# Kernel tuning notes

Hardware: AMD Instinct MI355X
Metric: run time of the kernel (lower is better)

The kernel has to match this reference:

```python
import jax, jax.numpy as jnp
import numpy as np

N, T, D = 32, 64, 16
F = 512  # object_classes == feature dim after object_fc


def _gcn(x, adj, W, b):
    # Kipf GraphConvolution: adj @ (x @ W) + b
    return adj @ (x @ W) + b


def _norm_adj(a):
    d = jnp.sum(a, axis=1) ** -0.5
    return a * d[:, None] * d[None, :]


def _per_graph(x, gc1_W, gc1_b, gc2_W, gc2_b, gc3_W, gc3_b, gc4_W, gc4_b):
    # x: [D, F]
    # graph_generator / adj2: softmax-style similarity adjacency with D^{-1/2} norm
    s = x @ x.T                                   # [D, D]
    a = jnp.exp(s - jnp.max(s, axis=1, keepdims=True))
    adj = _norm_adj(a)
    # branch 1
    x1 = jax.nn.relu(_gcn(x, adj, gc1_W, gc1_b))
    x1 = _gcn(x1, adj, gc2_W, gc2_b)
    # branch 2 (adj_hat2 identical construction from x)
    y2 = jax.nn.relu(_gcn(x, adj, gc3_W, gc3_b))  # [D, 32]
    y22 = y2 @ y2.T
    nrm = jnp.sqrt(jnp.sum(y22 * y22, axis=1, keepdims=True))  # torch.norm(y22, 2, dim=1)
    adj3 = 1.0 + y22 / (nrm @ nrm.T)
    adj_hat3 = _norm_adj(adj3)
    y2 = _gcn(y2, adj_hat3, gc4_W, gc4_b)
    return (x1 + y2) * 0.5


def setup_inputs() -> dict:
    key = jax.random.key(0)
    ks = jax.random.split(key, 12)
    s = 0.02
    return {
        "object_raw": jax.random.normal(ks[0], (N * T * D, F), jnp.float32),
        "action_raw": jax.random.normal(ks[1], (N * T, F), jnp.float32),
        "W_obj": jax.random.normal(ks[2], (F, 512), jnp.float32) * s,
        "b_obj": jnp.zeros((512,), jnp.float32),
        "W_act": jax.random.normal(ks[3], (F, 512), jnp.float32) * s,
        "b_act": jnp.zeros((512,), jnp.float32),
        "gc1_W": jax.random.normal(ks[4], (512, 32), jnp.float32) * s,
        "gc1_b": jnp.zeros((32,), jnp.float32),
        "gc2_W": jax.random.normal(ks[5], (32, 512), jnp.float32) * s,
        "gc2_b": jnp.zeros((512,), jnp.float32),
        "gc3_W": jax.random.normal(ks[6], (512, 32), jnp.float32) * s,
        "gc3_b": jnp.zeros((32,), jnp.float32),
        "gc4_W": jax.random.normal(ks[7], (32, 512), jnp.float32) * s,
        "gc4_b": jnp.zeros((512,), jnp.float32),
        "fc1_W": jax.random.normal(ks[8], (512, 1024), jnp.float32) * s,
        "fc1_b": jnp.zeros((1024,), jnp.float32),
        "clf_W": jax.random.normal(ks[9], (1024, 500), jnp.float32) * s,
        "clf_b": jnp.zeros((500,), jnp.float32),
    }


def reference(object_raw, action_raw, W_obj, b_obj, W_act, b_act,
              gc1_W, gc1_b, gc2_W, gc2_b, gc3_W, gc3_b, gc4_W, gc4_b,
              fc1_W, fc1_b, clf_W, clf_b):
    obj = jax.nn.relu(object_raw @ W_obj + b_obj).reshape(N * T, D, 512)
    act = jax.nn.relu(action_raw @ W_act + b_act)           # [N*T, 512]
    obj = obj.at[:, D // 2].set(act)                         # overwrite middle frame
    graph = jax.vmap(lambda x: _per_graph(x, gc1_W, gc1_b, gc2_W, gc2_b,
                                          gc3_W, gc3_b, gc4_W, gc4_b))(obj)
    g = graph.reshape(N, T, D, 512).mean(axis=2)
    o = obj.reshape(N, T, D, 512).mean(axis=2)
    feat = (o + g) * 0.5                                     # graph_fusion == 'mean'
    c = jax.nn.relu(feat)                                    # dropout = identity (eval)
    c = jax.nn.relu(c @ fc1_W + fc1_b)
    out = (c @ clf_W + clf_b).mean(axis=1)                   # mean over T -> [N, 500]
    return out
```

## Files before the change

### kernel.cpp

```cpp
#include <hip/hip_runtime.h>
#include <hip/hip_bf16.h>

using ushort_t = unsigned short;
using f32x4  = __attribute__((ext_vector_type(4))) float;
using short8 = __attribute__((ext_vector_type(8))) short;

__device__ __forceinline__ float bflo(unsigned p) {
    union { unsigned u; float f; } x; x.u = p << 16; return x.f;
}
__device__ __forceinline__ float bfhi(unsigned p) {
    union { unsigned u; float f; } x; x.u = p & 0xffff0000u; return x.f;
}
__device__ __forceinline__ ushort_t f2bf(float f) {
    __hip_bfloat16 h = __float2bfloat16(f);
    return *(ushort_t*)&h;
}
__device__ __forceinline__ unsigned pk2bf(float lo, float hi) {
    __hip_bfloat162 h = __float22bfloat162_rn({lo, hi});
    return *(unsigned*)&h;
}

__device__ __forceinline__ void tr_tile(const float* __restrict__ S, ushort_t* __restrict__ D,
                                        int K, int N, int Npad, int bx, int by,
                                        int tx, int ty, float* tile )
{
    const int k0 = by * 32, n0 = bx * 32;
#pragma unroll
    for (int r = 0; r < 4; r++) {
        const int k = k0 + ty + r * 8, n = n0 + tx;
        tile[(ty + r * 8) * 33 + tx] = (k < K && n < N) ? S[(size_t)k * N + n] : 0.f;
    }
    __syncthreads();
#pragma unroll
    for (int r = 0; r < 4; r++) {
        const int n = n0 + ty + r * 8, k = k0 + tx;
        if (n < Npad && k < K) D[(size_t)n * K + k] = f2bf(tile[tx * 33 + ty + r * 8]);
    }
}

__global__ __launch_bounds__(256)
void prep_weights(const float* __restrict__ Wobj, ushort_t* __restrict__ WobjT,
                  const float* __restrict__ Wact, ushort_t* __restrict__ WactT,
                  const float* __restrict__ fc1W, ushort_t* __restrict__ fc1T,
                  const float* __restrict__ gc1W, ushort_t* __restrict__ W1t,
                  const float* __restrict__ gc3W, ushort_t* __restrict__ W3t,
                  const float* __restrict__ gc2W, ushort_t* __restrict__ W2bf,
                  const float* __restrict__ gc4W, ushort_t* __restrict__ W4bf)
{
    __shared__ float tile[32 * 33];
    const int b = blockIdx.x;
    const int t = threadIdx.x;
    const int tx = t & 31, ty = t >> 5;

    if (b < 1056) {
        const float* S; ushort_t* D; int K, N, Npad, nt, l;
        if      (b < 256)  { S = Wobj; D = WobjT; K = 512; N = 512;  Npad = 512;  nt = 16; l = b; }
        else if (b < 512)  { S = Wact; D = WactT; K = 512; N = 512;  Npad = 512;  nt = 16; l = b - 256; }
        else if (b < 1024) { S = fc1W; D = fc1T;  K = 512; N = 1024; Npad = 1024; nt = 32; l = b - 512; }
        else if (b < 1040) { S = gc1W; D = W1t;   K = 512; N = 32;   Npad = 32;   nt = 1;  l = b - 1024; }
        else               { S = gc3W; D = W3t;   K = 512; N = 32;   Npad = 32;   nt = 1;  l = b - 1040; }
        tr_tile(S, D, K, N, Npad, l % nt, l / nt, tx, ty, tile);
    } else {
        const float* S = (b < 1064) ? gc2W : gc4W;
        ushort_t* D    = (b < 1064) ? W2bf : W4bf;
        const int i = (b < 1064 ? b - 1056 : b - 1064) * 256 + t;
        const float4 x = ((const float4*)S)[2 * i];
        const float4 y = ((const float4*)S)[2 * i + 1];
        unsigned r[4] = { pk2bf(x.x, x.y), pk2bf(x.z, x.w), pk2bf(y.x, y.y), pk2bf(y.z, y.w) };
        ((uint4*)D)[i] = *(uint4*)r;
    }
}

__global__ __launch_bounds__(512, 4)
void gemm_obj_stream(const float* __restrict__ A, const ushort_t* __restrict__ Bt,
                     const float* __restrict__ bias, ushort_t* __restrict__ C)
{
    __shared__ __align__(16) ushort_t As[64 * 512];
    const int t = threadIdx.x;
    const int lane = t & 63, w = t >> 6;
    const int bm = blockIdx.x * 64;
    const int fr = lane & 15, fq = lane >> 4;

#pragma unroll
    for (int i = 0; i < 8; i++) {
        const int flat = i * 512 + t;
        const int row = flat >> 6, c = flat & 63;
        const float* gp = A + (size_t)(bm + row) * 512 + c * 8;
        const float4 p0 = *(const float4*)gp;
        const float4 p1 = *(const float4*)(gp + 4);
        unsigned rr[4] = { pk2bf(p0.x, p0.y), pk2bf(p0.z, p0.w),
                           pk2bf(p1.x, p1.y), pk2bf(p1.z, p1.w) };
        *(uint4*)&As[row * 512 + ((c ^ (row & 7)) * 8)] = *(uint4*)rr;
    }
    __syncthreads();

    const int nw = w * 64;
    const ushort_t* Bbase = Bt + (size_t)(nw + fr) * 512 + fq * 8;

    f32x4 acc[4][4];
#pragma unroll
    for (int j = 0; j < 4; j++)
#pragma unroll
        for (int i = 0; i < 4; i++) acc[j][i] = (f32x4){0.f, 0.f, 0.f, 0.f};

    uint4 bA[4], bB[4];
#pragma unroll
    for (int j = 0; j < 4; j++) bA[j] = *(const uint4*)(Bbase + (size_t)j * 16 * 512);

    for (int kk = 0; kk < 16; kk += 2) {
        short8 af[4];
#pragma unroll
        for (int i = 0; i < 4; i++)
            af[i] = *(const short8*)&As[(i * 16 + fr) * 512 + (((kk * 4 + fq) ^ (fr & 7)) * 8)];
#pragma unroll
        for (int j = 0; j < 4; j++) {
            bB[j] = *(const uint4*)(Bbase + (size_t)j * 16 * 512 + (kk + 1) * 32);
            const short8 bf = *(const short8*)&bA[j];
#pragma unroll
            for (int i = 0; i < 4; i++)
                acc[j][i] = __builtin_amdgcn_mfma_f32_16x16x32_bf16(af[i], bf, acc[j][i], 0, 0, 0);
        }
#pragma unroll
        for (int i = 0; i < 4; i++)
            af[i] = *(const short8*)&As[(i * 16 + fr) * 512 + ((((kk + 1) * 4 + fq) ^ (fr & 7)) * 8)];
#pragma unroll
        for (int j = 0; j < 4; j++) {
            if (kk + 2 < 16)
                bA[j] = *(const uint4*)(Bbase + (size_t)j * 16 * 512 + (kk + 2) * 32);
            const short8 bf = *(const short8*)&bB[j];
#pragma unroll
            for (int i = 0; i < 4; i++)
                acc[j][i] = __builtin_amdgcn_mfma_f32_16x16x32_bf16(af[i], bf, acc[j][i], 0, 0, 0);
        }
    }

#pragma unroll
    for (int j = 0; j < 4; j++) {
        const int n = nw + j * 16 + fr;
        const float bv = bias[n];
#pragma unroll
        for (int i = 0; i < 4; i++) {
#pragma unroll
            for (int rr = 0; rr < 4; rr++) {
                const int ml = fq * 4 + rr;
                if (ml == 8) continue;
                const int m = bm + i * 16 + ml;
                C[(size_t)m * 512 + n] = f2bf(fmaxf(acc[j][i][rr] + bv, 0.f));
            }
        }
    }
}

typedef __attribute__((address_space(1))) void glb_void;
typedef __attribute__((address_space(3))) void lds_void;
__device__ __forceinline__ void dma16(const void* g, void* l) {
    __builtin_amdgcn_global_load_lds((glb_void*)(unsigned long long)(uintptr_t)g,
                                     (lds_void*)(unsigned)(uintptr_t)l, 16, 0, 0);
}

template<int RELU, typename AT>
__global__ __launch_bounds__(256)
void gemm_dma(const AT* __restrict__ A, const ushort_t* __restrict__ Bt,
              const float* __restrict__ bias, ushort_t* __restrict__ C,
              int N, int K, int Nb, int row_mul, int row_add)
{
    __shared__ __align__(16) char     AsRaw[128 * 32 * sizeof(AT)];
    __shared__ __align__(16) ushort_t Bs[128 * 32];
    const int t = threadIdx.x;
    const int lane = t & 63, w = t >> 6;
    const int bm = blockIdx.y * 128, bn = blockIdx.x * 128;
    const int mb = (w & 1) * 64, nb = (w >> 1) * 64;
    const int fr = lane & 15, fq = lane >> 4;

    f32x4 acc[16];
#pragma unroll
    for (int i = 0; i < 16; i++) acc[i] = (f32x4){0.f, 0.f, 0.f, 0.f};

    const int brow = lane >> 2, bk = lane & 3;
    const int klog = bk ^ ((brow >> 1) & 3);
    const int arow = lane >> 3, ag = lane & 7;

    for (int k0 = 0; k0 < K; k0 += 32) {
        __syncthreads();
        if constexpr (sizeof(AT) == 4) {
#pragma unroll
            for (int i = 0; i < 4; i++) {
                const int grp = w * 4 + i;
                const int row = grp * 8 + arow;
                const int gl = ag ^ (row & 7);
                dma16((const float*)A + (size_t)(bm + row) * K + k0 + gl * 4,
                      AsRaw + grp * 1024);
            }
        } else {
#pragma unroll
            for (int i = 0; i < 2; i++) {
                const int grp = w * 2 + i;
                const int row = grp * 16 + brow;
                dma16((const ushort_t*)A + (size_t)(bm + row) * K + k0 + klog * 8,
                      (ushort_t*)AsRaw + grp * 512);
            }
        }
#pragma unroll
        for (int i = 0; i < 2; i++) {
            const int grp = w * 2 + i;
            const int row = grp * 16 + brow;
            dma16(Bt + (size_t)(bn + row) * K + k0 + klog * 8, Bs + grp * 512);
        }
        __syncthreads();

        short8 af[4], bf[4];
        if constexpr (sizeof(AT) == 4) {
#pragma unroll
            for (int i = 0; i < 4; i++) {
                const int row = mb + i * 16 + fr;
                const float* base = (const float*)AsRaw + row * 32;
                const f32x4 p0 = *(const f32x4*)(base + (((2 * fq)     ^ (fr & 7)) * 4));
                const f32x4 p1 = *(const f32x4*)(base + (((2 * fq + 1) ^ (fr & 7)) * 4));
                unsigned rr[4] = { pk2bf(p0.x, p0.y), pk2bf(p0.z, p0.w),
                                   pk2bf(p1.x, p1.y), pk2bf(p1.z, p1.w) };
                af[i] = *(short8*)rr;
            }
        } else {
#pragma unroll
            for (int i = 0; i < 4; i++) {
                const int row = mb + i * 16 + fr;
                af[i] = *(const short8*)((const ushort_t*)AsRaw + row * 32 + (fq ^ ((fr >> 1) & 3)) * 8);
            }
        }
#pragma unroll
        for (int j = 0; j < 4; j++) {
            const int row = nb + j * 16 + fr;
            bf[j] = *(const short8*)(Bs + row * 32 + (fq ^ ((fr >> 1) & 3)) * 8);
        }
#pragma unroll
        for (int i = 0; i < 4; i++)
#pragma unroll
            for (int j = 0; j < 4; j++)
                acc[i * 4 + j] = __builtin_amdgcn_mfma_f32_16x16x32_bf16(
                    af[i], bf[j], acc[i * 4 + j], 0, 0, 0);
    }

#pragma unroll
    for (int j = 0; j < 4; j++) {
        const int n = bn + nb + j * 16 + fr;
        const float bv = (n < Nb) ? bias[n] : 0.f;
#pragma unroll
        for (int i = 0; i < 4; i++) {
            const f32x4 a = acc[i * 4 + j];
#pragma unroll
            for (int r = 0; r < 4; r++) {
                const int m = bm + mb + i * 16 + fq * 4 + r;
                float v = a[r] + bv;
                if (RELU) v = fmaxf(v, 0.f);
                C[((size_t)m * row_mul + row_add) * (size_t)N + n] = f2bf(v);
            }
        }
    }
}

__global__ __launch_bounds__(64)
void graph_mfma(const ushort_t* __restrict__ obj,
                const ushort_t* __restrict__ W1t, const float* __restrict__ b1,
                const ushort_t* __restrict__ W2b, const float* __restrict__ b2,
                const ushort_t* __restrict__ W3t, const float* __restrict__ b3,
                const ushort_t* __restrict__ W4b, const float* __restrict__ b4,
                ushort_t* __restrict__ cbuf)
{
    __shared__ float ssb[16 * 17];
    __shared__ float adjt[16 * 20];
    __shared__ float t1s[16 * 36];
    __shared__ float t3s[16 * 36];
    __shared__ float x1s[16 * 36];
    __shared__ float y2s[16 * 36];
    __shared__ float y22s[16 * 17];
    __shared__ float a3t[16 * 20];
    __shared__ float dv[16], dv3[16], nrm[16], cA[16], cA3[16];
    __shared__ float zc1[32], zc4[32];

    const int lane = threadIdx.x;
    const int r = lane & 15, fq = lane >> 4;
    const ushort_t* xg = obj + (size_t)blockIdx.x * 8192;

    short8 xf[16];
#pragma unroll
    for (int kk = 0; kk < 16; kk++)
        xf[kk] = *(const short8*)(xg + r * 512 + kk * 32 + fq * 8);

    f32x4 sacc = (f32x4){0.f, 0.f, 0.f, 0.f};
#pragma unroll
    for (int kk = 0; kk < 16; kk++)
        sacc = __builtin_amdgcn_mfma_f32_16x16x32_bf16(xf[kk], xf[kk], sacc, 0, 0, 0);

    f32x4 a10 = (f32x4){0.f,0.f,0.f,0.f}, a11 = a10, a30 = a10, a31 = a10;
#pragma unroll
    for (int kk = 0; kk < 16; kk++) {
        const short8 w10 = *(const short8*)(W1t + (size_t)(r)      * 512 + kk * 32 + fq * 8);
        const short8 w11 = *(const short8*)(W1t + (size_t)(16 + r) * 512 + kk * 32 + fq * 8);
        const short8 w30 = *(const short8*)(W3t + (size_t)(r)      * 512 + kk * 32 + fq * 8);
        const short8 w31 = *(const short8*)(W3t + (size_t)(16 + r) * 512 + kk * 32 + fq * 8);
        a10 = __builtin_amdgcn_mfma_f32_16x16x32_bf16(xf[kk], w10, a10, 0, 0, 0);
        a11 = __builtin_amdgcn_mfma_f32_16x16x32_bf16(xf[kk], w11, a11, 0, 0, 0);
        a30 = __builtin_amdgcn_mfma_f32_16x16x32_bf16(xf[kk], w30, a30, 0, 0, 0);
        a31 = __builtin_amdgcn_mfma_f32_16x16x32_bf16(xf[kk], w31, a31, 0, 0, 0);
    }

#pragma unroll
    for (int i = 0; i < 4; i++) {
        const int m = fq * 4 + i;
        ssb[m * 17 + r] = sacc[i];
        t1s[m * 36 + r]      = a10[i];
        t1s[m * 36 + 16 + r] = a11[i];
        t3s[m * 36 + r]      = a30[i];
        t3s[m * 36 + 16 + r] = a31[i];
    }
    __syncthreads();

    if (lane < 16) {
        float m = ssb[lane * 17];
#pragma unroll
        for (int j = 1; j < 16; j++) m = fmaxf(m, ssb[lane * 17 + j]);
        float s = 0.f;
#pragma unroll
        for (int j = 0; j < 16; j++) {
            const float e = expf(ssb[lane * 17 + j] - m);
            ssb[lane * 17 + j] = e; s += e;
        }
        dv[lane] = rsqrtf(s);
    }
    __syncthreads();

    {
        const float di = dv[r];
#pragma unroll
        for (int p = 0; p < 4; p++) {
            const int j = fq * 4 + p;
            adjt[j * 20 + r] = ssb[r * 17 + j] * di * dv[j];
        }
    }
    __syncthreads();

    if (lane < 16) {
        float s = 0.f;
#pragma unroll
        for (int i = 0; i < 16; i++) s += adjt[lane * 20 + i];
        cA[lane] = s;
    }

    {
        const int c = lane & 31, hi = lane >> 5;
        const float bb1 = b1[c], bb3 = b3[c];
        float ax[8], ay[8];
#pragma unroll
        for (int i = 0; i < 8; i++) { ax[i] = bb1; ay[i] = bb3; }
#pragma unroll
        for (int j = 0; j < 16; j++) {
            const float t1v = t1s[j * 36 + c], t3v = t3s[j * 36 + c];
            const float4 p = *(const float4*)&adjt[j * 20 + hi * 8];
            const float4 q = *(const float4*)&adjt[j * 20 + hi * 8 + 4];
            ax[0] = fmaf(p.x, t1v, ax[0]); ax[1] = fmaf(p.y, t1v, ax[1]);
            ax[2] = fmaf(p.z, t1v, ax[2]); ax[3] = fmaf(p.w, t1v, ax[3]);
            ax[4] = fmaf(q.x, t1v, ax[4]); ax[5] = fmaf(q.y, t1v, ax[5]);
            ax[6] = fmaf(q.z, t1v, ax[6]); ax[7] = fmaf(q.w, t1v, ax[7]);
            ay[0] = fmaf(p.x, t3v, ay[0]); ay[1] = fmaf(p.y, t3v, ay[1]);
            ay[2] = fmaf(p.z, t3v, ay[2]); ay[3] = fmaf(p.w, t3v, ay[3]);
            ay[4] = fmaf(q.x, t3v, ay[4]); ay[5] = fmaf(q.y, t3v, ay[5]);
            ay[6] = fmaf(q.z, t3v, ay[6]); ay[7] = fmaf(q.w, t3v, ay[7]);
        }
#pragma unroll
        for (int i = 0; i < 8; i++) {
            x1s[(hi * 8 + i) * 36 + c] = fmaxf(ax[i], 0.f);
            y2s[(hi * 8 + i) * 36 + c] = fmaxf(ay[i], 0.f);
        }
    }
    __syncthreads();

    {
        const int i2 = lane >> 2, j0 = (lane & 3) * 4;
        float a4[4] = {0.f, 0.f, 0.f, 0.f};
#pragma unroll
        for (int k4 = 0; k4 < 8; k4++) {
            const float4 yi = *(const float4*)&y2s[i2 * 36 + k4 * 4];
#pragma unroll
            for (int p = 0; p < 4; p++) {
                const float4 yj = *(const float4*)&y2s[(j0 + p) * 36 + k4 * 4];
                a4[p] = fmaf(yi.x, yj.x, a4[p]); a4[p] = fmaf(yi.y, yj.y, a4[p]);
                a4[p] = fmaf(yi.z, yj.z, a4[p]); a4[p] = fmaf(yi.w, yj.w, a4[p]);
            }
        }
#pragma unroll
        for (int p = 0; p < 4; p++) y22s[i2 * 17 + j0 + p] = a4[p];
    }
    __syncthreads();

    if (lane < 16) {
        float sq = 0.f;
#pragma unroll
        for (int j = 0; j < 16; j++) { const float v = y22s[lane * 17 + j]; sq = fmaf(v, v, sq); }
        nrm[lane] = sqrtf(sq);
    }
    __syncthreads();

    {
        const float ni = nrm[r];
#pragma unroll
        for (int p = 0; p < 4; p++) {
            const int j = fq * 4 + p;
            a3t[j * 20 + r] = 1.0f + y22s[r * 17 + j] / (ni * nrm[j]);
        }
    }
    __syncthreads();

    if (lane < 16) {
        float s = 0.f;
#pragma unroll
        for (int j = 0; j < 16; j++) s += a3t[j * 20 + lane];
        dv3[lane] = rsqrtf(s);
    }
    __syncthreads();

    if (lane < 16) {
        float s = 0.f;
#pragma unroll
        for (int i = 0; i < 16; i++) s = fmaf(a3t[lane * 20 + i], dv3[i], s);
        cA3[lane] = s * dv3[lane];
    }
    __syncthreads();

    if (lane < 32) {
        float s1 = 0.f, s4 = 0.f;
#pragma unroll
        for (int j = 0; j < 16; j++) {
            s1 = fmaf(cA[j],  x1s[j * 36 + lane], s1);
            s4 = fmaf(cA3[j], y2s[j * 36 + lane], s4);
        }
        zc1[lane] = s1; zc4[lane] = s4;
    }
    __syncthreads();

    {
        float om[8] = {0,0,0,0,0,0,0,0};
#pragma unroll
        for (int m = 0; m < 16; m++) {
            const uint4 q = *(const uint4*)(xg + m * 512 + lane * 8);
            om[0] += bflo(q.x); om[1] += bfhi(q.x);
            om[2] += bflo(q.y); om[3] += bfhi(q.y);
            om[4] += bflo(q.z); om[5] += bfhi(q.z);
            om[6] += bflo(q.w); om[7] += bfhi(q.w);
        }
        float gm[8] = {0,0,0,0,0,0,0,0};
        for (int k = 0; k < 32; k++) {
            const float z1 = zc1[k], z4 = zc4[k];
            const uint4 w2 = *(const uint4*)(W2b + (size_t)k * 512 + lane * 8);
            const uint4 w4 = *(const uint4*)(W4b + (size_t)k * 512 + lane * 8);
            gm[0] = fmaf(z1, bflo(w2.x), gm[0]); gm[0] = fmaf(z4, bflo(w4.x), gm[0]);
            gm[1] = fmaf(z1, bfhi(w2.x), gm[1]); gm[1] = fmaf(z4, bfhi(w4.x), gm[1]);
            gm[2] = fmaf(z1, bflo(w2.y), gm[2]); gm[2] = fmaf(z4, bflo(w4.y), gm[2]);
            gm[3] = fmaf(z1, bfhi(w2.y), gm[3]); gm[3] = fmaf(z4, bfhi(w4.y), gm[3]);
            gm[4] = fmaf(z1, bflo(w2.z), gm[4]); gm[4] = fmaf(z4, bflo(w4.z), gm[4]);
            gm[5] = fmaf(z1, bfhi(w2.z), gm[5]); gm[5] = fmaf(z4, bfhi(w4.z), gm[5]);
            gm[6] = fmaf(z1, bflo(w2.w), gm[6]); gm[6] = fmaf(z4, bflo(w4.w), gm[6]);
            gm[7] = fmaf(z1, bfhi(w2.w), gm[7]); gm[7] = fmaf(z4, bfhi(w4.w), gm[7]);
        }
        const float4 b2a = *(const float4*)&b2[lane * 8];
        const float4 b2b = *(const float4*)&b2[lane * 8 + 4];
        const float4 b4a = *(const float4*)&b4[lane * 8];
        const float4 b4b = *(const float4*)&b4[lane * 8 + 4];
        const float bs[8] = { b2a.x + b4a.x, b2a.y + b4a.y, b2a.z + b4a.z, b2a.w + b4a.w,
                              b2b.x + b4b.x, b2b.y + b4b.y, b2b.z + b4b.z, b2b.w + b4b.w };
        ushort_t pk[8];
#pragma unroll
        for (int c = 0; c < 8; c++) {
            const float gmean = 0.5f * bs[c] + gm[c] * (1.0f / 32.0f);
            const float feat  = 0.5f * (om[c] * 0.0625f + gmean);
            pk[c] = f2bf(fmaxf(feat, 0.f));
        }
        *(uint4*)(cbuf + (size_t)blockIdx.x * 512 + lane * 8) = *(uint4*)pk;
    }
}

__global__ __launch_bounds__(256)
void mean_c2(const ushort_t* __restrict__ c2, float* __restrict__ cmean)
{
    const int idx = blockIdx.x * 256 + threadIdx.x;
    const int n = idx >> 10, k = idx & 1023;
    const ushort_t* p = c2 + (size_t)n * 64 * 1024 + k;
    float s = 0.f;
#pragma unroll 8
    for (int tt = 0; tt < 64; tt++) {
        union { unsigned u; float f; } x; x.u = ((unsigned)p[tt * 1024]) << 16;
        s += x.f;
    }
    cmean[idx] = s * (1.0f / 64.0f);
}

__global__ __launch_bounds__(256)
void clf_col(const float* __restrict__ cmean, const float* __restrict__ W,
             const float* __restrict__ clf_b, float* __restrict__ out)
{
    __shared__ float red[8][33];
    const int j = blockIdx.x;
    const int t = threadIdx.x;
    const int n = t & 31, kp = t >> 5;
    const float* cm = cmean + (size_t)n * 1024 + kp * 128;
    const float* wp = W + (size_t)kp * 128 * 500 + j;
    float acc = 0.f;
#pragma unroll
    for (int k = 0; k < 128; k += 4) {
        const float4 c = *(const float4*)(cm + k);
        acc = fmaf(c.x, wp[(size_t)(k + 0) * 500], acc);
        acc = fmaf(c.y, wp[(size_t)(k + 1) * 500], acc);
        acc = fmaf(c.z, wp[(size_t)(k + 2) * 500], acc);
        acc = fmaf(c.w, wp[(size_t)(k + 3) * 500], acc);
    }
    red[kp][n] = acc;
    __syncthreads();
    if (t < 32) {
        float s = red[0][t];
#pragma unroll
        for (int p = 1; p < 8; p++) s += red[p][t];
        out[(size_t)t * 500 + j] = s + clf_b[j];
    }
}

extern "C" void kernel_launch(void* const* d_in, const int* in_sizes, int n_in,
                              void* d_out, int out_size, void* d_ws, size_t ws_size,
                              hipStream_t stream)
{
    const float* object_raw = (const float*)d_in[0];
    const float* action_raw = (const float*)d_in[1];
    const float* W_obj = (const float*)d_in[2];
    const float* b_obj = (const float*)d_in[3];
    const float* W_act = (const float*)d_in[4];
    const float* b_act = (const float*)d_in[5];
    const float* gc1_W = (const float*)d_in[6];
    const float* gc1_b = (const float*)d_in[7];
    const float* gc2_W = (const float*)d_in[8];
    const float* gc2_b = (const float*)d_in[9];
    const float* gc3_W = (const float*)d_in[10];
    const float* gc3_b = (const float*)d_in[11];
    const float* gc4_W = (const float*)d_in[12];
    const float* gc4_b = (const float*)d_in[13];
    const float* fc1_W = (const float*)d_in[14];
    const float* fc1_b = (const float*)d_in[15];
    const float* clf_W = (const float*)d_in[16];
    const float* clf_b = (const float*)d_in[17];

    char* ws = (char*)d_ws;
    const size_t MB = 1024 * 1024;
    ushort_t* obj_bf = (ushort_t*)(ws);
    ushort_t* cbuf   = (ushort_t*)(ws + 32 * MB);
    ushort_t* c2     = (ushort_t*)(ws + 34 * MB);
    float*    cmean  = (float*)   (ws + 38 * MB);
    ushort_t* WobjT  = (ushort_t*)(ws + 39 * MB);
    ushort_t* WactT  = (ushort_t*)(ws + 39 * MB + 512 * 1024);
    ushort_t* fc1T   = (ushort_t*)(ws + 40 * MB);
    ushort_t* W1t    = (ushort_t*)(ws + 41 * MB);
    ushort_t* W3t    = (ushort_t*)(ws + 41 * MB + 32 * 1024);
    ushort_t* W2bf   = (ushort_t*)(ws + 41 * MB + 64 * 1024);
    ushort_t* W4bf   = (ushort_t*)(ws + 41 * MB + 96 * 1024);

    prep_weights<<<dim3(1072), 256, 0, stream>>>(
        W_obj, WobjT, W_act, WactT, fc1_W, fc1T,
        gc1_W, W1t, gc3_W, W3t, gc2_W, W2bf, gc4_W, W4bf);

    gemm_obj_stream<<<dim3(512), 512, 0, stream>>>(object_raw, WobjT, b_obj, obj_bf);

    gemm_dma<1, float><<<dim3(4, 16), 256, 0, stream>>>(
        action_raw, WactT, b_act, obj_bf, 512, 512, 512, 16, 8);

    graph_mfma<<<dim3(2048), 64, 0, stream>>>(
        obj_bf, W1t, gc1_b, W2bf, gc2_b, W3t, gc3_b, W4bf, gc4_b, cbuf);

    gemm_dma<1, ushort_t><<<dim3(8, 16), 256, 0, stream>>>(
        cbuf, fc1T, fc1_b, c2, 1024, 512, 1024, 1, 0);

    mean_c2<<<dim3(128), 256, 0, stream>>>(c2, cmean);

    clf_col<<<dim3(500), 256, 0, stream>>>(cmean, clf_W, clf_b, (float*)d_out);
}
```

Baseline: 247.4 us.

## Double M tile of object GEMM and stage epilogue through LDS for coalesced stores

The streaming object-projection GEMM now processes 128 rows per block instead of 64, with 8 accumulator tiles per wave. Each loaded weight fragment is therefore reused across twice as many rows, and the grid is halved to 256 blocks. The epilogue writes bias+ReLU results into the reused LDS buffer with an XOR swizzle, then emits 16-byte coalesced row stores instead of scattered 2-byte stores. The first B prefetch is also hoisted above the barrier. In exchange, LDS use doubles to 128KB per block, occupancy drops to one block per CU, and the middle-frame rows are now written too and later overwritten by the action GEMM.

```diff
diff --git a/kernel.cpp b/kernel.cpp
--- a/kernel.cpp
+++ b/kernel.cpp
@@ -71,57 +71,58 @@
     }
 }
 
-__global__ __launch_bounds__(512, 4)
+__global__ __launch_bounds__(512, 2)
 void gemm_obj_stream(const float* __restrict__ A, const ushort_t* __restrict__ Bt,
                      const float* __restrict__ bias, ushort_t* __restrict__ C)
 {
-    __shared__ __align__(16) ushort_t As[64 * 512];
+    __shared__ __align__(16) ushort_t As[128 * 512];
     const int t = threadIdx.x;
     const int lane = t & 63, w = t >> 6;
-    const int bm = blockIdx.x * 64;
+    const int bm = blockIdx.x * 128;
     const int fr = lane & 15, fq = lane >> 4;
 
-#pragma unroll
-    for (int i = 0; i < 8; i++) {
-        const int flat = i * 512 + t;
-        const int row = flat >> 6, c = flat & 63;
-        const float* gp = A + (size_t)(bm + row) * 512 + c * 8;
-        const float4 p0 = *(const float4*)gp;
-        const float4 p1 = *(const float4*)(gp + 4);
+    const float4* A4 = (const float4*)(A + (size_t)bm * 512);
+#pragma unroll
+    for (int i = 0; i < 16; i++) {
+        const int fl = i * 1024 + t * 2;
+        const int row = fl >> 7;
+        const float4 p0 = A4[fl];
+        const float4 p1 = A4[fl + 1];
         unsigned rr[4] = { pk2bf(p0.x, p0.y), pk2bf(p0.z, p0.w),
                            pk2bf(p1.x, p1.y), pk2bf(p1.z, p1.w) };
-        *(uint4*)&As[row * 512 + ((c ^ (row & 7)) * 8)] = *(uint4*)rr;
-    }
-    __syncthreads();
+        *(uint4*)&As[row * 512 + ((lane ^ (row & 7)) * 8)] = *(uint4*)rr;
+    }
 
     const int nw = w * 64;
     const ushort_t* Bbase = Bt + (size_t)(nw + fr) * 512 + fq * 8;
 
-    f32x4 acc[4][4];
+    uint4 bA[4], bB[4];
+#pragma unroll
+    for (int j = 0; j < 4; j++) bA[j] = *(const uint4*)(Bbase + (size_t)j * 16 * 512);
+
+    __syncthreads();
+
+    f32x4 acc[4][8];
 #pragma unroll
     for (int j = 0; j < 4; j++)
 #pragma unroll
-        for (int i = 0; i < 4; i++) acc[j][i] = (f32x4){0.f, 0.f, 0.f, 0.f};
-
-    uint4 bA[4], bB[4];
-#pragma unroll
-    for (int j = 0; j < 4; j++) bA[j] = *(const uint4*)(Bbase + (size_t)j * 16 * 512);
+        for (int i = 0; i < 8; i++) acc[j][i] = (f32x4){0.f, 0.f, 0.f, 0.f};
 
     for (int kk = 0; kk < 16; kk += 2) {
-        short8 af[4];
-#pragma unroll
-        for (int i = 0; i < 4; i++)
+        short8 af[8];
+#pragma unroll
+        for (int i = 0; i < 8; i++)
             af[i] = *(const short8*)&As[(i * 16 + fr) * 512 + (((kk * 4 + fq) ^ (fr & 7)) * 8)];
 #pragma unroll
         for (int j = 0; j < 4; j++) {
             bB[j] = *(const uint4*)(Bbase + (size_t)j * 16 * 512 + (kk + 1) * 32);
             const short8 bf = *(const short8*)&bA[j];
 #pragma unroll
-            for (int i = 0; i < 4; i++)
+            for (int i = 0; i < 8; i++)
                 acc[j][i] = __builtin_amdgcn_mfma_f32_16x16x32_bf16(af[i], bf, acc[j][i], 0, 0, 0);
         }
 #pragma unroll
-        for (int i = 0; i < 4; i++)
+        for (int i = 0; i < 8; i++)
             af[i] = *(const short8*)&As[(i * 16 + fr) * 512 + ((((kk + 1) * 4 + fq) ^ (fr & 7)) * 8)];
 #pragma unroll
         for (int j = 0; j < 4; j++) {
@@ -129,25 +130,36 @@
                 bA[j] = *(const uint4*)(Bbase + (size_t)j * 16 * 512 + (kk + 2) * 32);
             const short8 bf = *(const short8*)&bB[j];
 #pragma unroll
-            for (int i = 0; i < 4; i++)
+            for (int i = 0; i < 8; i++)
                 acc[j][i] = __builtin_amdgcn_mfma_f32_16x16x32_bf16(af[i], bf, acc[j][i], 0, 0, 0);
         }
     }
 
+    __syncthreads();
 #pragma unroll
     for (int j = 0; j < 4; j++) {
-        const int n = nw + j * 16 + fr;
-        const float bv = bias[n];
-#pragma unroll
-        for (int i = 0; i < 4; i++) {
-#pragma unroll
-            for (int rr = 0; rr < 4; rr++) {
-                const int ml = fq * 4 + rr;
-                if (ml == 8) continue;
-                const int m = bm + i * 16 + ml;
-                C[(size_t)m * 512 + n] = f2bf(fmaxf(acc[j][i][rr] + bv, 0.f));
-            }
-        }
+        const int col0 = j * 16 + fr;
+        const float bv = bias[nw + col0];
+#pragma unroll
+        for (int i = 0; i < 8; i++) {
+#pragma unroll
+            for (int rr2 = 0; rr2 < 4; rr2++) {
+                const int m = i * 16 + fq * 4 + rr2;
+                const int pc = col0 ^ (((m >> 2) & 3) << 4);
+                As[m * 512 + nw + pc] = f2bf(fmaxf(acc[j][i][rr2] + bv, 0.f));
+            }
+        }
+    }
+    __syncthreads();
+#pragma unroll
+    for (int i2 = 0; i2 < 16; i2++) {
+        const int fl = i2 * 512 + t;
+        const int m  = fl >> 6;
+        const int n0 = (fl & 63) * 8;
+        const int sl = n0 & ~63;
+        const int cl = n0 & 63;
+        const uint4 v = *(const uint4*)&As[m * 512 + sl + (cl ^ (((m >> 2) & 3) << 4))];
+        *(uint4*)&C[(size_t)(bm + m) * 512 + n0] = v;
     }
 }
 
@@ -563,7 +575,7 @@
         W_obj, WobjT, W_act, WactT, fc1_W, fc1T,
         gc1_W, W1t, gc3_W, W3t, gc2_W, W2bf, gc4_W, W4bf);
 
-    gemm_obj_stream<<<dim3(512), 512, 0, stream>>>(object_raw, WobjT, b_obj, obj_bf);
+    gemm_obj_stream<<<dim3(256), 512, 0, stream>>>(object_raw, WobjT, b_obj, obj_bf);
 
     gemm_dma<1, float><<<dim3(4, 16), 256, 0, stream>>>(
         action_raw, WactT, b_act, obj_bf, 512, 512, 512, 16, 8);
```

Measured after the change: 241.8 us. 2.3% less time.
